# Performance work log

Hardware: AMD Instinct MI355X
Metric: run time of the kernel (lower is better)

The kernel has to match this reference:

```python
import jax, jax.numpy as jnp
import numpy as np
import math

N, LQ, D, H, L, P, DFF, NL = 16, 300, 256, 8, 3, 4, 1024, 6
TLENS = (4096, 2048, 1024)
T = sum(TLENS)
TEMP = 10000.0

def _ln(x, g, b, eps=1e-5):
    m = x.mean(-1, keepdims=True)
    v = ((x - m) ** 2).mean(-1, keepdims=True)
    return (x - m) * jax.lax.rsqrt(v + eps) * g + b

def _mlp2(x, w0, b0, w1, b1):
    return jax.nn.relu(x @ w0.T + b0) @ w1.T + b1

def _sine_embed(ref):
    # ref: (N, LQ, 2) (center, width) -> (N, LQ, 2*D)
    dim_t = TEMP ** (2.0 * (jnp.arange(D) // 2) / D)
    p = ref * (2.0 * math.pi)
    def inter(v):
        return jnp.stack([jnp.sin(v[..., 0::2]), jnp.cos(v[..., 1::2])], -1).reshape(v.shape[:-1] + (-1,))
    pc = p[..., 0:1] / dim_t
    pw = p[..., 1:2] / dim_t
    return jnp.concatenate([inter(pc), inter(pw)], -1)

def _mha(q, k, v, in_w, in_b, out_w, out_b):
    Nb, Lq, Dm = q.shape
    Dh = Dm // H
    wq, wk, wv = jnp.split(in_w, 3, 0)
    bq, bk, bv = jnp.split(in_b, 3, 0)
    qh = (q @ wq.T + bq).reshape(Nb, Lq, H, Dh)
    kh = (k @ wk.T + bk).reshape(Nb, Lq, H, Dh)
    vh = (v @ wv.T + bv).reshape(Nb, Lq, H, Dh)
    att = jax.nn.softmax(jnp.einsum('nqhd,nkhd->nhqk', qh, kh) / math.sqrt(Dh), -1)
    o = jnp.einsum('nhqk,nkhd->nqhd', att, vh).reshape(Nb, Lq, Dm)
    return o @ out_w.T + out_b

def _deform_attn(q, ref, src, pad_mask, t_lens, start, ow, ob, aww, awb, vw, vb, pw, pb):
    # q: (N,LQ,D); ref: (N,LQ,L,2) normalized (center,width); src: (N,T,D)
    Nb, Lq, Dm = q.shape
    Dh = Dm // H
    val = (src @ vw.T + vb) * (~pad_mask)[..., None]
    val = val.reshape(Nb, -1, H, Dh).transpose(0, 2, 1, 3)  # (N,H,T,Dh)
    off = (q @ ow.T + ob).reshape(Nb, Lq, H, L, P)
    aw = jax.nn.softmax((q @ aww.T + awb).reshape(Nb, Lq, H, L * P), -1).reshape(Nb, Lq, H, L, P)
    # 1-D deformable sampling locations: center + offset/P * width * 0.5
    loc = ref[:, :, None, :, 0, None] + off / P * ref[:, :, None, :, 1, None] * 0.5  # (N,LQ,H,L,P)
    tl = t_lens[None, None, None, :, None]
    x = loc * tl.astype(loc.dtype) - 0.5  # align_corners=False linear sampling
    x0f = jnp.floor(x)
    f = x - x0f
    x0 = x0f.astype(jnp.int32)
    m0 = (x0 >= 0) & (x0 < tl)
    m1 = (x0 + 1 >= 0) & (x0 + 1 < tl)
    st = start[None, None, None, :, None]
    i0 = st + jnp.clip(x0, 0, tl - 1)
    i1 = st + jnp.clip(x0 + 1, 0, tl - 1)
    def tr(a):
        return a.transpose(0, 2, 1, 3, 4).reshape(Nb, H, Lq * L * P)
    g0 = jnp.take_along_axis(val, tr(i0)[..., None], axis=2)  # (N,H,M,Dh)
    g1 = jnp.take_along_axis(val, tr(i1)[..., None], axis=2)
    samp = g0 * ((1.0 - tr(f)) * tr(m0))[..., None] + g1 * (tr(f) * tr(m1))[..., None]
    samp = samp.reshape(Nb, H, Lq, L * P, Dh)
    w = tr(aw).reshape(Nb, H, Lq, L * P)
    o = jnp.einsum('nhqk,nhqkd->nqhd', w, samp).reshape(Nb, Lq, Dm)
    return o @ pw.T + pb

def _forward(tgt, enc_output_segments, feature_durations, src, src_valid_ratios,
             grid_w0, grid_b0, grid_w1, grid_b1, qs_w0, qs_b0, qs_w1, qs_b1,
             sa_in_w, sa_in_b, sa_out_w, sa_out_b,
             n1_g, n1_b, n2_g, n2_b, n3_g, n3_b,
             off_w, off_b, aw_w, aw_b, val_w, val_b, outp_w, outp_b,
             ffn_w1, ffn_b1, ffn_w2, ffn_b2,
             temporal_lens, level_start_index, src_padding_mask):
    seg = jax.lax.stop_gradient(enc_output_segments)  # original detaches proposals
    ref = jnp.stack([seg[..., 0], jnp.exp(seg[..., 1])], -1)  # (N,LQ,2) center,width
    out = tgt
    for l in range(NL):
        ref_in = (ref / feature_durations[:, None, None])[:, :, None, :] * src_valid_ratios[:, None, :, None]
        sine = _sine_embed(ref)
        raw_qpos = _mlp2(sine, grid_w0, grid_b0, grid_w1, grid_b1)
        qpos = _mlp2(out, qs_w0, qs_b0, qs_w1, qs_b1) * raw_qpos
        q = out + qpos
        out = _ln(out + _mha(q, q, out, sa_in_w[l], sa_in_b[l], sa_out_w[l], sa_out_b[l]), n1_g[l], n1_b[l])
        ca = _deform_attn(out + qpos, ref_in, src, src_padding_mask, temporal_lens, level_start_index,
                          off_w[l], off_b[l], aw_w[l], aw_b[l], val_w[l], val_b[l], outp_w[l], outp_b[l])
        out = _ln(out + ca, n2_g[l], n2_b[l])
        ff = jax.nn.relu(out @ ffn_w1[l].T + ffn_b1[l]) @ ffn_w2[l].T + ffn_b2[l]
        out = _ln(out + ff, n3_g[l], n3_b[l])
    return out

def setup_inputs():
    key = jax.random.key(0)
    ks = iter(jax.random.split(key, 64))
    def nrm(shape, s=0.02):
        return (s * jax.random.normal(next(ks), shape)).astype(jnp.float32)
    dur = 64.0
    inp = {}
    inp['tgt'] = nrm((N, LQ, D), 1.0)
    c = jax.random.uniform(next(ks), (N, LQ)) * dur
    w = jnp.log(jax.random.uniform(next(ks), (N, LQ)) * 4.0 + 0.5)
    inp['enc_output_segments'] = jnp.stack([c, w], -1)
    inp['feature_durations'] = jnp.full((N,), dur, jnp.float32)
    inp['src'] = nrm((N, T, D), 1.0)
    inp['temporal_lens'] = jnp.array(TLENS, jnp.int32)
    inp['level_start_index'] = jnp.array(np.cumsum((0,) + TLENS[:-1]), jnp.int32)
    inp['src_valid_ratios'] = jnp.ones((N, L), jnp.float32)
    inp['src_padding_mask'] = jnp.zeros((N, T), bool)
    inp['grid_w0'] = nrm((D, 2 * D)); inp['grid_b0'] = jnp.zeros((D,))
    inp['grid_w1'] = nrm((D, D)); inp['grid_b1'] = jnp.zeros((D,))
    inp['qs_w0'] = nrm((D, D)); inp['qs_b0'] = jnp.zeros((D,))
    inp['qs_w1'] = nrm((D, D)); inp['qs_b1'] = jnp.zeros((D,))
    inp['sa_in_w'] = nrm((NL, 3 * D, D)); inp['sa_in_b'] = jnp.zeros((NL, 3 * D))
    inp['sa_out_w'] = nrm((NL, D, D)); inp['sa_out_b'] = jnp.zeros((NL, D))
    for nm in ('n1', 'n2', 'n3'):
        inp[nm + '_g'] = jnp.ones((NL, D)); inp[nm + '_b'] = jnp.zeros((NL, D))
    inp['off_w'] = nrm((NL, H * L * P, D))
    inp['off_b'] = (jax.random.uniform(next(ks), (NL, H * L * P)) * 2.0 - 1.0) * P
    inp['aw_w'] = nrm((NL, H * L * P, D)); inp['aw_b'] = jnp.zeros((NL, H * L * P))
    inp['val_w'] = nrm((NL, D, D)); inp['val_b'] = jnp.zeros((NL, D))
    inp['outp_w'] = nrm((NL, D, D)); inp['outp_b'] = jnp.zeros((NL, D))
    inp['ffn_w1'] = nrm((NL, DFF, D)); inp['ffn_b1'] = jnp.zeros((NL, DFF))
    inp['ffn_w2'] = nrm((NL, D, DFF)); inp['ffn_b2'] = jnp.zeros((NL, D))
    return inp

def reference(tgt, enc_output_segments, feature_durations, src, temporal_lens, level_start_index,
              src_valid_ratios, src_padding_mask,
              grid_w0, grid_b0, grid_w1, grid_b1, qs_w0, qs_b0, qs_w1, qs_b1,
              sa_in_w, sa_in_b, sa_out_w, sa_out_b,
              n1_g, n1_b, n2_g, n2_b, n3_g, n3_b,
              off_w, off_b, aw_w, aw_b, val_w, val_b, outp_w, outp_b,
              ffn_w1, ffn_b1, ffn_w2, ffn_b2):
    return _forward(tgt, enc_output_segments, feature_durations, src, src_valid_ratios,
                    grid_w0, grid_b0, grid_w1, grid_b1, qs_w0, qs_b0, qs_w1, qs_b1,
                    sa_in_w, sa_in_b, sa_out_w, sa_out_b,
                    n1_g, n1_b, n2_g, n2_b, n3_g, n3_b,
                    off_w, off_b, aw_w, aw_b, val_w, val_b, outp_w, outp_b,
                    ffn_w1, ffn_b1, ffn_w2, ffn_b2,
                    temporal_lens, level_start_index, src_padding_mask)
```

## Files before the change

kernel.cpp:

```cpp
#include <hip/hip_runtime.h>
#include <cstdint>

#define NB   16
#define LQN  300
#define DM   256
#define NH   8
#define DH   32
#define NLV  3
#define DFFN 1024
#define NLAY 6
#define TT   7168
#define MROW (NB*LQN)
#define SROW (NB*TT)

typedef __attribute__((ext_vector_type(8))) short bf16x8;
typedef __attribute__((ext_vector_type(4))) float f32x4;

__device__ __forceinline__ float bf2f(short u) {
  unsigned x = ((unsigned)(unsigned short)u) << 16;
  return __builtin_bit_cast(float, x);
}
__device__ __forceinline__ short f2bf(float f) {
  unsigned u = __builtin_bit_cast(unsigned, f);
  u += 0x7fffu + ((u >> 16) & 1u);
  return (short)(u >> 16);
}
__device__ __forceinline__ void load_lds16(const void* g, void* l) {
  __builtin_amdgcn_global_load_lds(
      (const __attribute__((address_space(1))) unsigned int*)g,
      (__attribute__((address_space(3))) unsigned int*)l, 16, 0, 0);
}
#define MFMA(a,b,c) __builtin_amdgcn_mfma_f32_16x16x32_bf16((a),(b),(c),0,0,0)

struct CvtPtrs { const float* p[13]; };

__global__ __launch_bounds__(256)
void cvt_all_kernel(CvtPtrs ptrs, short* __restrict__ dst)
{
  const long gid = (long)blockIdx.x*256 + threadIdx.x;
  const long cums[14] = {0,32768,49152,65536,81920,376832,475136,512000,
                         548864,647168,745472,1138688,1531904,8871936};
  int s = 0;
  #pragma unroll
  for (int i = 1; i < 13; ++i) s += (gid >= cums[i]) ? 1 : 0;
  const long rel = gid - cums[s];
  const float4 v = ((const float4*)ptrs.p[s])[rel];
  long dstIdx = gid;
  if (s == 6) { const long l = rel/6144, w = rel%6144; dstIdx = 475136 + l*12288 + w; }
  else if (s == 7) { const long l = rel/6144, w = rel%6144; dstIdx = 475136 + l*12288 + 6144 + w; }
  ((short4*)dst)[dstIdx] = make_short4(f2bf(v.x), f2bf(v.y), f2bf(v.z), f2bf(v.w));
}

#define VLS 264

__global__ __launch_bounds__(512, 1)
void val_gemm(const short* __restrict__ srcbf, const short* __restrict__ Bw,
              const float* __restrict__ bias, short* __restrict__ Cb,
              const unsigned char* __restrict__ rowmask)
{
  __shared__ short Bs[256*VLS];
  const int tid = threadIdx.x, wid = tid >> 6, lane = tid & 63;
  const int fr = lane & 15, fq = lane >> 4;

  for (int t = tid; t < 8192; t += 512) {
    const int row = t >> 5, ch = t & 31;
    const int chs = ch ^ ((row >> 4) & 7);
    *(bf16x8*)&Bs[row*VLS + chs*8] = *(const bf16x8*)(Bw + row*256 + ch*8);
  }
  __syncthreads();

  float bv[16];
  #pragma unroll
  for (int j = 0; j < 4; ++j)
    *(float4*)&bv[j*4] = *(const float4*)(bias + fr*16 + j*4);

  const int rbase = (blockIdx.x*8 + wid) * 32;

  bf16x8 a[2][8];
  #pragma unroll
  for (int h = 0; h < 2; ++h)
    #pragma unroll
    for (int ks = 0; ks < 8; ++ks)
      a[h][ks] = *(const bf16x8*)(srcbf + (long)(rbase + h*16 + fr)*256 + ks*32 + fq*8);

  f32x4 acc[2][16] = {};
  #pragma unroll
  for (int ks = 0; ks < 8; ++ks) {
    #pragma unroll
    for (int nt = 0; nt < 16; ++nt) {
      const bf16x8 b = *(const bf16x8*)&Bs[(fr*16 + nt)*VLS + (((ks*4 + fq) ^ (fr & 7)))*8];
      acc[0][nt] = MFMA(a[0][ks], b, acc[0][nt]);
      acc[1][nt] = MFMA(a[1][ks], b, acc[1][nt]);
    }
  }

  #pragma unroll
  for (int h = 0; h < 2; ++h) {
    #pragma unroll
    for (int r = 0; r < 4; ++r) {
      const int grow = rbase + h*16 + fq*4 + r;
      const float msc = rowmask[grow] ? 0.0f : 1.0f;
      bf16x8 o0, o1;
      #pragma unroll
      for (int j = 0; j < 8; ++j) {
        o0[j] = f2bf((acc[h][j][r]   + bv[j])   * msc);
        o1[j] = f2bf((acc[h][8+j][r] + bv[8+j]) * msc);
      }
      short* cp = Cb + (long)grow*256 + fr*16;
      *(bf16x8*)cp       = o0;
      *(bf16x8*)(cp + 8) = o1;
    }
  }
}

template<int EPI>
__global__ __launch_bounds__(256)
void gemm64(const short* __restrict__ A, const short* __restrict__ B,
            const float* __restrict__ bias, const float* __restrict__ bias2,
            float* __restrict__ Cf, short* __restrict__ Cb, short* __restrict__ Cb2,
            int M, int N, int K, int ldc,
            const float* __restrict__ rawq, const float* __restrict__ resid)
{
  __shared__ short As[2][64*64];
  __shared__ short Bs[2][64*64];
  const int tid = threadIdx.x, wid = tid >> 6, lane = tid & 63;
  const int wr = wid >> 1, wc = wid & 1;
  const int fr = lane & 15, fq = lane >> 4;
  const int bm = blockIdx.x, bn = blockIdx.y;
  const int lrow = lane >> 3;
  const int schk = ((lane & 7) ^ lrow) * 8;
  const int nk = K >> 6;

  f32x4 acc[2][2] = {};

  auto stg = [&](int kt, int bsel) {
    const int k0 = kt << 6;
    #pragma unroll
    for (int i = 0; i < 2; ++i) {
      const int rr = wid*16 + i*8 + lrow;
      load_lds16(A + (long)(bm*64 + rr)*K + k0 + schk, &As[bsel][(wid*16 + i*8)*64]);
      load_lds16(B + (long)(bn*64 + rr)*K + k0 + schk, &Bs[bsel][(wid*16 + i*8)*64]);
    }
  };

  stg(0, 0);
  for (int t = 0; t < nk; ++t) {
    const int cur = t & 1;
    if (t + 1 < nk) {
      stg(t + 1, cur ^ 1);
      asm volatile("s_waitcnt vmcnt(4)" ::: "memory");
    } else {
      asm volatile("s_waitcnt vmcnt(0)" ::: "memory");
    }
    __builtin_amdgcn_s_barrier();
    __builtin_amdgcn_sched_barrier(0);
    #pragma unroll
    for (int kk = 0; kk < 64; kk += 32) {
      bf16x8 af[2], bv[2];
      #pragma unroll
      for (int mi = 0; mi < 2; ++mi)
        af[mi] = *(const bf16x8*)&As[cur][(wr*32 + mi*16 + fr)*64 + (((kk>>3)+fq) ^ (fr&7))*8];
      #pragma unroll
      for (int ni = 0; ni < 2; ++ni)
        bv[ni] = *(const bf16x8*)&Bs[cur][(wc*32 + ni*16 + fr)*64 + (((kk>>3)+fq) ^ (fr&7))*8];
      #pragma unroll
      for (int mi = 0; mi < 2; ++mi)
        #pragma unroll
        for (int ni = 0; ni < 2; ++ni)
          acc[mi][ni] = MFMA(af[mi], bv[ni], acc[mi][ni]);
    }
    __builtin_amdgcn_s_barrier();
  }

  #pragma unroll
  for (int mi = 0; mi < 2; ++mi) {
    #pragma unroll
    for (int r = 0; r < 4; ++r) {
      const int grow = bm*64 + wr*32 + mi*16 + fq*4 + r;
      #pragma unroll
      for (int ni = 0; ni < 2; ++ni) {
        const int gcol = bn*64 + wc*32 + ni*16 + fr;
        float v = acc[mi][ni][r];
        if (EPI == 4) v += (gcol < 96) ? bias[gcol] : bias2[gcol-96];
        else v += bias[gcol];
        const long off = (long)grow*ldc + gcol;
        if (EPI == 0) {
          if (Cf) Cf[off] = v;
          if (Cb) Cb[off] = f2bf(v);
        } else if (EPI == 1) {
          Cb[off] = f2bf(fmaxf(v, 0.0f));
        } else if (EPI == 2) {
          const float qp = v * rawq[off];
          Cf[off] = qp;
          Cb[off] = f2bf(resid[off] + qp);
        } else if (EPI == 4) {
          Cf[off] = v;
        }
      }
    }
  }
}

__global__ __launch_bounds__(256)
void ew0_kernel(const float* __restrict__ tgt, float* __restrict__ out, short* __restrict__ outbf)
{
  const long i = (long)blockIdx.x*256 + threadIdx.x;
  const float4 v = ((const float4*)tgt)[i];
  ((float4*)out)[i] = v;
  ((short4*)outbf)[i] = make_short4(f2bf(v.x), f2bf(v.y), f2bf(v.z), f2bf(v.w));
}

__global__ __launch_bounds__(256)
void init_ref_kernel(const float* __restrict__ seg, const float* __restrict__ dur,
                     const float* __restrict__ valid,
                     short* __restrict__ sinebf, float* __restrict__ refin)
{
  const int m = blockIdx.x;
  const int n = m / LQN;
  const int t = threadIdx.x;
  const float c = seg[(long)m*2 + 0];
  const float w = __expf(seg[(long)m*2 + 1]);
  const float e = (float)(t & ~1) * (1.0f/256.0f);
  const float invdim = __expf(-e * 9.2103403719761836f);
  const float twopi = 6.2831853071795864f;
  const float a0 = c * twopi * invdim;
  const float a1 = w * twopi * invdim;
  const float v0 = (t & 1) ? cosf(a0) : sinf(a0);
  const float v1 = (t & 1) ? cosf(a1) : sinf(a1);
  sinebf[(long)m*512 + t]       = f2bf(v0);
  sinebf[(long)m*512 + 256 + t] = f2bf(v1);
  if (t < 6) {
    const int l = t >> 1, cc = t & 1;
    const float rv = cc ? w : c;
    refin[(long)m*6 + l*2 + cc] = rv / dur[n] * valid[n*NLV + l];
  }
}

#define KPAD 320
#define KSTR 40
#define VSTR 328
#define PSTR 328

__global__ __launch_bounds__(256)
void attn_mfma(const short* __restrict__ qk, const short* __restrict__ vv,
               short* __restrict__ outb)
{
  __shared__ short Kl[KPAD*KSTR];
  __shared__ short Vt[DH*VSTR];
  __shared__ short Pl[4][16*PSTR];
  const int b = blockIdx.x;
  const int half = b & 1, h = (b >> 1) & 7, n = b >> 4;
  const int tid = threadIdx.x, wid = tid >> 6, lane = tid & 63;
  const int fr = lane & 15, fq = lane >> 4;

  const short* qkn = qk + (long)n*LQN*512;
  const short* vn  = vv + (long)n*LQN*256;

  for (int t = tid; t < KPAD*4; t += 256) {
    const int r = t >> 2, c = t & 3;
    bf16x8 kv = {}, vw = {};
    if (r < LQN) {
      kv = *(const bf16x8*)(qkn + (long)r*512 + 256 + h*32 + c*8);
      vw = *(const bf16x8*)(vn  + (long)r*256 + h*32 + c*8);
    }
    *(bf16x8*)&Kl[r*KSTR + c*8] = kv;
    #pragma unroll
    for (int j = 0; j < 8; ++j) Vt[(c*8+j)*VSTR + r] = vw[j];
  }
  for (int t = tid; t < 4*16*24; t += 256) {
    const int w = t / (16*24), rr = (t / 24) & 15, cc = t % 24;
    Pl[w][rr*PSTR + 304 + cc] = 0;
  }
  __syncthreads();

  const int tlo = half ? 10 : 0, thi = half ? 19 : 10;
  const float scl2 = 0.17677669529663687f * 1.4426950408889634f;

  for (int qt = tlo + wid; qt < thi; qt += 4) {
    const int q0 = qt * 16;
    const int qrow = min(q0 + fr, LQN-1);
    const bf16x8 qf = *(const bf16x8*)(qkn + (long)qrow*512 + h*32 + fq*8);
    f32x4 s[19];
    #pragma unroll
    for (int t = 0; t < 19; ++t) {
      const bf16x8 kf = *(const bf16x8*)&Kl[(t*16+fr)*KSTR + fq*8];
      s[t] = MFMA(qf, kf, ((f32x4){0.f,0.f,0.f,0.f}));
    }
    float mx[4] = {-3e38f,-3e38f,-3e38f,-3e38f};
    #pragma unroll
    for (int t = 0; t < 19; ++t) {
      const bool valid = (t < 18) || (fr < 12);
      #pragma unroll
      for (int r = 0; r < 4; ++r) if (valid) mx[r] = fmaxf(mx[r], s[t][r]);
    }
    #pragma unroll
    for (int r = 0; r < 4; ++r) {
      #pragma unroll
      for (int o = 1; o < 16; o <<= 1) mx[r] = fmaxf(mx[r], __shfl_xor(mx[r], o));
      mx[r] *= scl2;
    }
    float l[4] = {0.f,0.f,0.f,0.f};
    #pragma unroll
    for (int t = 0; t < 19; ++t) {
      const bool valid = (t < 18) || (fr < 12);
      #pragma unroll
      for (int r = 0; r < 4; ++r) {
        const float p = valid ? exp2f(s[t][r]*scl2 - mx[r]) : 0.0f;
        l[r] += p;
        Pl[wid][(fq*4+r)*PSTR + t*16 + fr] = f2bf(p);
      }
    }
    #pragma unroll
    for (int r = 0; r < 4; ++r) {
      #pragma unroll
      for (int o = 1; o < 16; o <<= 1) l[r] += __shfl_xor(l[r], o);
    }
    f32x4 o0 = {}, o1 = {};
    #pragma unroll
    for (int ck = 0; ck < 10; ++ck) {
      const bf16x8 pf = *(const bf16x8*)&Pl[wid][fr*PSTR + ck*32 + fq*8];
      const bf16x8 v0 = *(const bf16x8*)&Vt[fr*VSTR + ck*32 + fq*8];
      const bf16x8 v1 = *(const bf16x8*)&Vt[(16+fr)*VSTR + ck*32 + fq*8];
      o0 = MFMA(pf, v0, o0);
      o1 = MFMA(pf, v1, o1);
    }
    #pragma unroll
    for (int r = 0; r < 4; ++r) {
      const int qq = q0 + fq*4 + r;
      if (qq < LQN) {
        const float inv = 1.0f / l[r];
        outb[((long)(n*LQN+qq))*256 + h*32 + fr]      = f2bf(o0[r]*inv);
        outb[((long)(n*LQN+qq))*256 + h*32 + 16 + fr] = f2bf(o1[r]*inv);
      }
    }
  }
}

__global__ __launch_bounds__(256)
void ln_kernel(const float* __restrict__ resid, const float* __restrict__ delta,
               const float* __restrict__ g, const float* __restrict__ b,
               float* __restrict__ of, short* __restrict__ ob,
               const float* __restrict__ qpos, short* __restrict__ caqb)
{
  const int m = blockIdx.x, c = threadIdx.x;
  const long idx = (long)m*DM + c;
  const float x = resid[idx] + delta[idx];
  float s = x, s2 = x*x;
  #pragma unroll
  for (int o = 1; o < 64; o <<= 1) { s += __shfl_xor(s, o); s2 += __shfl_xor(s2, o); }
  __shared__ float rs[4], rs2[4];
  const int w = c >> 6;
  if ((c & 63) == 0) { rs[w] = s; rs2[w] = s2; }
  __syncthreads();
  s  = rs[0]+rs[1]+rs[2]+rs[3];
  s2 = rs2[0]+rs2[1]+rs2[2]+rs2[3];
  const float mean = s * (1.0f/DM);
  const float var  = s2 * (1.0f/DM) - mean*mean;
  const float y = (x - mean) * rsqrtf(var + 1e-5f) * g[c] + b[c];
  of[idx] = y;
  if (ob) ob[idx] = f2bf(y);
  if (qpos) caqb[idx] = f2bf(y + qpos[idx]);
}

__global__ __launch_bounds__(256)
void sample_kernel(const short* __restrict__ val, int ldv,
                   const float* __restrict__ offaw, const float* __restrict__ refin,
                   const int* __restrict__ tlens, const int* __restrict__ lstart,
                   short* __restrict__ cab)
{
  const int m = blockIdx.x;
  const int n = m / LQN;
  const int tid = threadIdx.x;
  __shared__ int2  lI[96];
  __shared__ float2 lW[96];
  if ((tid & 31) == 0) {
    const int h = tid >> 5;
    const float* row = offaw + (long)m*192;
    float aw[12];
    float mx = -1e30f;
    #pragma unroll
    for (int lp = 0; lp < 12; ++lp) { aw[lp] = row[96 + h*12 + lp]; mx = fmaxf(mx, aw[lp]); }
    float sum = 0.0f;
    #pragma unroll
    for (int lp = 0; lp < 12; ++lp) { aw[lp] = __expf(aw[lp]-mx); sum += aw[lp]; }
    const float invs = 1.0f / sum;
    #pragma unroll
    for (int lp = 0; lp < 12; ++lp) {
      const int l = lp >> 2;
      const int tli = tlens[l];
      const float off = row[h*12 + lp];
      const float loc = refin[(long)m*6 + l*2] + off * 0.25f * refin[(long)m*6 + l*2 + 1] * 0.5f;
      const float x = loc * (float)tli - 0.5f;
      const float x0f = floorf(x);
      const float f = x - x0f;
      const int x0 = (int)x0f;
      const int i0 = lstart[l] + min(max(x0,   0), tli-1);
      const int i1 = lstart[l] + min(max(x0+1, 0), tli-1);
      const float wgt = aw[lp]*invs;
      const float w0 = (x0   >= 0 && x0   < tli) ? wgt*(1.0f-f) : 0.0f;
      const float w1 = (x0+1 >= 0 && x0+1 < tli) ? wgt*f        : 0.0f;
      lI[h*12 + lp] = make_int2(i0, i1);
      lW[h*12 + lp] = make_float2(w0, w1);
    }
  }
  __syncthreads();
  const int h = tid >> 5;
  const short* vb = val + (long)n*TT*ldv;
  float acc = 0.0f;
  #pragma unroll
  for (int lp = 0; lp < 12; ++lp) {
    const int e = h*12 + lp;
    const int2 ii = lI[e];
    const float2 ww = lW[e];
    acc += ww.x * bf2f(vb[(long)ii.x*ldv + tid]) + ww.y * bf2f(vb[(long)ii.y*ldv + tid]);
  }
  cab[(long)m*DM + tid] = f2bf(acc);
}

static inline void g64(hipStream_t st, int epi, const short* A, const short* B,
                       const float* bias, const float* bias2,
                       float* Cf, short* Cb, short* Cb2,
                       int M, int N, int K, int ldc,
                       const float* rawq = nullptr, const float* resid = nullptr)
{
  dim3 g(M/64, N/64), blk(256);
  switch (epi) {
    case 0: gemm64<0><<<g,blk,0,st>>>(A,B,bias,bias2,Cf,Cb,Cb2,M,N,K,ldc,rawq,resid); break;
    case 1: gemm64<1><<<g,blk,0,st>>>(A,B,bias,bias2,Cf,Cb,Cb2,M,N,K,ldc,rawq,resid); break;
    case 2: gemm64<2><<<g,blk,0,st>>>(A,B,bias,bias2,Cf,Cb,Cb2,M,N,K,ldc,rawq,resid); break;
    default:gemm64<4><<<g,blk,0,st>>>(A,B,bias,bias2,Cf,Cb,Cb2,M,N,K,ldc,rawq,resid); break;
  }
}

extern "C" void kernel_launch(void* const* d_in, const int* in_sizes, int n_in,
                              void* d_out, int out_size, void* d_ws, size_t ws_size,
                              hipStream_t stream)
{
  const float* tgt    = (const float*)d_in[0];
  const float* seg    = (const float*)d_in[1];
  const float* dur    = (const float*)d_in[2];
  const float* src    = (const float*)d_in[3];
  const int*   tlens  = (const int*)d_in[4];
  const int*   lstart = (const int*)d_in[5];
  const float* valid  = (const float*)d_in[6];
  const unsigned char* pmask = (const unsigned char*)d_in[7];
  const float* grid_w0 = (const float*)d_in[8];
  const float* grid_b0 = (const float*)d_in[9];
  const float* grid_w1 = (const float*)d_in[10];
  const float* grid_b1 = (const float*)d_in[11];
  const float* qs_w0 = (const float*)d_in[12];
  const float* qs_b0 = (const float*)d_in[13];
  const float* qs_w1 = (const float*)d_in[14];
  const float* qs_b1 = (const float*)d_in[15];
  const float* sa_in_w  = (const float*)d_in[16];
  const float* sa_in_b  = (const float*)d_in[17];
  const float* sa_out_w = (const float*)d_in[18];
  const float* sa_out_b = (const float*)d_in[19];
  const float* n1_g = (const float*)d_in[20];
  const float* n1_b = (const float*)d_in[21];
  const float* n2_g = (const float*)d_in[22];
  const float* n2_b = (const float*)d_in[23];
  const float* n3_g = (const float*)d_in[24];
  const float* n3_b = (const float*)d_in[25];
  const float* off_w = (const float*)d_in[26];
  const float* off_b = (const float*)d_in[27];
  const float* aw_w  = (const float*)d_in[28];
  const float* aw_b  = (const float*)d_in[29];
  const float* val_w = (const float*)d_in[30];
  const float* val_b = (const float*)d_in[31];
  const float* outp_w = (const float*)d_in[32];
  const float* outp_b = (const float*)d_in[33];
  const float* ffn_w1 = (const float*)d_in[34];
  const float* ffn_b1 = (const float*)d_in[35];
  const float* ffn_w2 = (const float*)d_in[36];
  const float* ffn_b2 = (const float*)d_in[37];

  const long W_G0=0, W_G1=131072, W_QS0=196608, W_QS1=262144, W_SAIN=327680,
             W_SAOUT=1507328, W_OFFAW=1900544, W_VAL=2195456,
             W_OUTP=2588672, W_FFN1=2981888, W_FFN2=4554752, W_SRC=6127616;

  char* ws = (char*)d_ws;
  short* wbf    = (short*)(ws + 0);
  short* srcbf  = wbf + W_SRC;
  short* sinebf = (short*)(ws + 70975488);
  short* ghbf   = (short*)(ws + 75890688);
  float* rawq   = (float*)(ws + 78348288);
  float* out    = (float*)(ws + 83263488);
  short* qbf    = (short*)(ws + 88178688);
  short* outbf  = qbf + (long)MROW*DM;
  short* t1bf   = (short*)(ws + 93093888);
  float* qpos   = (float*)(ws + 95551488);
  short* qkbf   = (short*)(ws + 100466688);
  short* vbf    = (short*)(ws + 105381888);
  short* attnbf = (short*)(ws + 107839488);
  float* tmpf   = (float*)(ws + 110297088);
  short* caqb   = (short*)(ws + 115212288);
  float* offaw  = (float*)(ws + 117669888);
  short* cabf   = (short*)(ws + 128729088);
  short* ffnhbf = (short*)(ws + 131186688);
  float* refin  = (float*)(ws + 141017088);
  short* valbf  = (short*)(ws + 141132288);

  CvtPtrs cp;
  cp.p[0]=grid_w0; cp.p[1]=grid_w1; cp.p[2]=qs_w0; cp.p[3]=qs_w1; cp.p[4]=sa_in_w;
  cp.p[5]=sa_out_w; cp.p[6]=off_w; cp.p[7]=aw_w; cp.p[8]=val_w; cp.p[9]=outp_w;
  cp.p[10]=ffn_w1; cp.p[11]=ffn_w2; cp.p[12]=src;
  cvt_all_kernel<<<dim3(34656), dim3(256), 0, stream>>>(cp, wbf);

  ew0_kernel<<<dim3(1200), dim3(256), 0, stream>>>(tgt, out, outbf);
  init_ref_kernel<<<dim3(MROW), dim3(256), 0, stream>>>(seg, dur, valid, sinebf, refin);

  g64(stream, 1, sinebf, wbf + W_G0, grid_b0, nullptr, nullptr, ghbf, nullptr, MROW, 256, 512, 256);
  g64(stream, 0, ghbf,   wbf + W_G1, grid_b1, nullptr, rawq, nullptr, nullptr, MROW, 256, 256, 256);

  for (int l = 0; l < NLAY; ++l) {
    g64(stream, 1, outbf, wbf + W_QS0, qs_b0, nullptr, nullptr, t1bf, nullptr, MROW, 256, 256, 256);
    g64(stream, 2, t1bf,  wbf + W_QS1, qs_b1, nullptr, qpos, qbf, nullptr, MROW, 256, 256, 256,
        rawq, out);
    g64(stream, 0, qbf, wbf + W_SAIN + (long)l*196608, sa_in_b + l*768, nullptr,
        nullptr, qkbf, nullptr, MROW, 512, 256, 512);
    g64(stream, 0, outbf, wbf + W_SAIN + (long)l*196608 + 131072, sa_in_b + l*768 + 512, nullptr,
        nullptr, vbf, nullptr, MROW, 256, 256, 256);
    attn_mfma<<<dim3(256), dim3(256), 0, stream>>>(qkbf, vbf, attnbf);
    g64(stream, 0, attnbf, wbf + W_SAOUT + (long)l*65536, sa_out_b + l*256, nullptr,
        tmpf, nullptr, nullptr, MROW, 256, 256, 256);
    ln_kernel<<<dim3(MROW), dim3(256), 0, stream>>>(out, tmpf, n1_g + l*256, n1_b + l*256,
                                                    out, outbf, qpos, caqb);
    g64(stream, 4, caqb, wbf + W_OFFAW + (long)l*49152, off_b + l*96, aw_b + l*96,
        offaw, nullptr, nullptr, MROW, 192, 256, 192);
    val_gemm<<<dim3(448), dim3(512), 0, stream>>>(
        srcbf, wbf + W_VAL + (long)l*65536, val_b + l*256, valbf, pmask);
    sample_kernel<<<dim3(MROW), dim3(256), 0, stream>>>(
        valbf, 256, offaw, refin, tlens, lstart, cabf);
    g64(stream, 0, cabf, wbf + W_OUTP + (long)l*65536, outp_b + l*256, nullptr,
        tmpf, nullptr, nullptr, MROW, 256, 256, 256);
    ln_kernel<<<dim3(MROW), dim3(256), 0, stream>>>(out, tmpf, n2_g + l*256, n2_b + l*256,
                                                    out, outbf, nullptr, nullptr);
    g64(stream, 1, outbf, wbf + W_FFN1 + (long)l*262144, ffn_b1 + l*1024, nullptr,
        nullptr, ffnhbf, nullptr, MROW, 1024, 256, 1024);
    g64(stream, 0, ffnhbf, wbf + W_FFN2 + (long)l*262144, ffn_b2 + l*256, nullptr,
        tmpf, nullptr, nullptr, MROW, 256, 1024, 256);
    float* of = (l == NLAY-1) ? (float*)d_out : out;
    ln_kernel<<<dim3(MROW), dim3(256), 0, stream>>>(out, tmpf, n3_g + l*256, n3_b + l*256,
                                                    of, outbf, nullptr, nullptr);
  }
}
```

Baseline: 996.3 us.

## Replace K=256 GEMMs with weight-stationary LDS kernel holding full B slice

Adds an sgemm kernel that loads a whole 256-column by 256-K weight slice into shared memory once per block. Each wave then computes a 16-row strip with A held in registers and writes vectorized epilogues. All K=256 projections move to this kernel, while the K=512/1024 GEMMs stay on a simplified gemm64. The aim is to cut the repeated K-loop staging and barriers and to widen stores. In exchange it uses large LDS (about 128KB+ per block), gives one block per CU, and needs many accumulator registers.

```diff
diff --git a/kernel.cpp b/kernel.cpp
--- a/kernel.cpp
+++ b/kernel.cpp
@@ -114,12 +114,120 @@
 }
 
 template<int EPI>
+__global__ __launch_bounds__(512, 1)
+void sgemm(const short* __restrict__ A, const short* __restrict__ Bw,
+           const float* __restrict__ bias, const float* __restrict__ bias2,
+           float* __restrict__ Cf, short* __restrict__ Cb,
+           int M, int NR, int ldc,
+           const float* __restrict__ rawq, const float* __restrict__ resid)
+{
+  __shared__ short Bs[256*VLS];
+  const int tid = threadIdx.x, wid = tid >> 6, lane = tid & 63;
+  const int fr = lane & 15, fq = lane >> 4;
+  const int coff = blockIdx.y * 256;
+
+  for (int t = tid; t < NR*32; t += 512) {
+    const int row = t >> 5, ch = t & 31;
+    const int chs = ch ^ ((row >> 4) & 7);
+    *(bf16x8*)&Bs[row*VLS + chs*8] = *(const bf16x8*)(Bw + (long)(coff + row)*256 + ch*8);
+  }
+  __syncthreads();
+
+  const int s = blockIdx.x*8 + wid;
+  if (s*16 >= M) return;
+  const int rbase = s*16;
+  const bool colok = (fr*16 < NR);
+
+  float bv[16];
+  if (colok) {
+    #pragma unroll
+    for (int j = 0; j < 16; ++j) {
+      const int gc = coff + fr*16 + j;
+      if (EPI == 4) bv[j] = (gc < 96) ? bias[gc] : bias2[gc - 96];
+      else          bv[j] = bias[gc];
+    }
+  } else {
+    #pragma unroll
+    for (int j = 0; j < 16; ++j) bv[j] = 0.0f;
+  }
+
+  bf16x8 a[8];
+  #pragma unroll
+  for (int ks = 0; ks < 8; ++ks)
+    a[ks] = *(const bf16x8*)(A + (long)(rbase + fr)*256 + ks*32 + fq*8);
+
+  f32x4 acc[16] = {};
+  #pragma unroll
+  for (int ks = 0; ks < 8; ++ks)
+    #pragma unroll
+    for (int nt = 0; nt < 16; ++nt) {
+      const bf16x8 b = *(const bf16x8*)&Bs[(fr*16 + nt)*VLS + (((ks*4 + fq) ^ (fr & 7)))*8];
+      acc[nt] = MFMA(a[ks], b, acc[nt]);
+    }
+
+  if (!colok) return;
+
+  #pragma unroll
+  for (int r = 0; r < 4; ++r) {
+    const int grow = rbase + fq*4 + r;
+    const long off = (long)grow*ldc + coff + fr*16;
+    float y[16];
+    #pragma unroll
+    for (int nt = 0; nt < 16; ++nt) y[nt] = acc[nt][r] + bv[nt];
+
+    if (EPI == 0) {
+      if (Cf) {
+        #pragma unroll
+        for (int j = 0; j < 4; ++j) *(float4*)(Cf + off + j*4) = *(const float4*)&y[j*4];
+      }
+      if (Cb) {
+        bf16x8 o0, o1;
+        #pragma unroll
+        for (int j = 0; j < 8; ++j) { o0[j] = f2bf(y[j]); o1[j] = f2bf(y[8+j]); }
+        *(bf16x8*)(Cb + off) = o0;
+        *(bf16x8*)(Cb + off + 8) = o1;
+      }
+    } else if (EPI == 1) {
+      bf16x8 o0, o1;
+      #pragma unroll
+      for (int j = 0; j < 8; ++j) {
+        o0[j] = f2bf(fmaxf(y[j],   0.0f));
+        o1[j] = f2bf(fmaxf(y[8+j], 0.0f));
+      }
+      *(bf16x8*)(Cb + off) = o0;
+      *(bf16x8*)(Cb + off + 8) = o1;
+    } else if (EPI == 2) {
+      float rq[16], rs[16];
+      #pragma unroll
+      for (int j = 0; j < 4; ++j) {
+        *(float4*)&rq[j*4] = *(const float4*)(rawq  + off + j*4);
+        *(float4*)&rs[j*4] = *(const float4*)(resid + off + j*4);
+      }
+      bf16x8 o0, o1;
+      #pragma unroll
+      for (int j = 0; j < 16; ++j) {
+        const float qp = y[j] * rq[j];
+        y[j] = qp;
+        const short b = f2bf(rs[j] + qp);
+        if (j < 8) o0[j] = b; else o1[j-8] = b;
+      }
+      #pragma unroll
+      for (int j = 0; j < 4; ++j) *(float4*)(Cf + off + j*4) = *(const float4*)&y[j*4];
+      *(bf16x8*)(Cb + off) = o0;
+      *(bf16x8*)(Cb + off + 8) = o1;
+    } else {
+      #pragma unroll
+      for (int j = 0; j < 4; ++j) *(float4*)(Cf + off + j*4) = *(const float4*)&y[j*4];
+    }
+  }
+}
+
+template<int EPI>
 __global__ __launch_bounds__(256)
 void gemm64(const short* __restrict__ A, const short* __restrict__ B,
-            const float* __restrict__ bias, const float* __restrict__ bias2,
-            float* __restrict__ Cf, short* __restrict__ Cb, short* __restrict__ Cb2,
-            int M, int N, int K, int ldc,
-            const float* __restrict__ rawq, const float* __restrict__ resid)
+            const float* __restrict__ bias,
+            float* __restrict__ Cf, short* __restrict__ Cb,
+            int M, int N, int K, int ldc)
 {
   __shared__ short As[2][64*64];
   __shared__ short Bs[2][64*64];
@@ -180,22 +288,10 @@
       #pragma unroll
       for (int ni = 0; ni < 2; ++ni) {
         const int gcol = bn*64 + wc*32 + ni*16 + fr;
-        float v = acc[mi][ni][r];
-        if (EPI == 4) v += (gcol < 96) ? bias[gcol] : bias2[gcol-96];
-        else v += bias[gcol];
+        const float v = acc[mi][ni][r] + bias[gcol];
         const long off = (long)grow*ldc + gcol;
-        if (EPI == 0) {
-          if (Cf) Cf[off] = v;
-          if (Cb) Cb[off] = f2bf(v);
-        } else if (EPI == 1) {
-          Cb[off] = f2bf(fmaxf(v, 0.0f));
-        } else if (EPI == 2) {
-          const float qp = v * rawq[off];
-          Cf[off] = qp;
-          Cb[off] = f2bf(resid[off] + qp);
-        } else if (EPI == 4) {
-          Cf[off] = v;
-        }
+        if (EPI == 0) Cf[off] = v;
+        else Cb[off] = f2bf(fmaxf(v, 0.0f));
       }
     }
   }
@@ -417,18 +513,17 @@
   cab[(long)m*DM + tid] = f2bf(acc);
 }
 
-static inline void g64(hipStream_t st, int epi, const short* A, const short* B,
-                       const float* bias, const float* bias2,
-                       float* Cf, short* Cb, short* Cb2,
-                       int M, int N, int K, int ldc,
-                       const float* rawq = nullptr, const float* resid = nullptr)
-{
-  dim3 g(M/64, N/64), blk(256);
+static inline void sg(hipStream_t st, int epi, const short* A, const short* B,
+                      const float* bias, const float* bias2,
+                      float* Cf, short* Cb, int M, int NR, int nbn, int ldc,
+                      const float* rawq = nullptr, const float* resid = nullptr)
+{
+  dim3 g((M/16 + 7)/8, nbn), blk(512);
   switch (epi) {
-    case 0: gemm64<0><<<g,blk,0,st>>>(A,B,bias,bias2,Cf,Cb,Cb2,M,N,K,ldc,rawq,resid); break;
-    case 1: gemm64<1><<<g,blk,0,st>>>(A,B,bias,bias2,Cf,Cb,Cb2,M,N,K,ldc,rawq,resid); break;
-    case 2: gemm64<2><<<g,blk,0,st>>>(A,B,bias,bias2,Cf,Cb,Cb2,M,N,K,ldc,rawq,resid); break;
-    default:gemm64<4><<<g,blk,0,st>>>(A,B,bias,bias2,Cf,Cb,Cb2,M,N,K,ldc,rawq,resid); break;
+    case 0: sgemm<0><<<g,blk,0,st>>>(A,B,bias,bias2,Cf,Cb,M,NR,ldc,rawq,resid); break;
+    case 1: sgemm<1><<<g,blk,0,st>>>(A,B,bias,bias2,Cf,Cb,M,NR,ldc,rawq,resid); break;
+    case 2: sgemm<2><<<g,blk,0,st>>>(A,B,bias,bias2,Cf,Cb,M,NR,ldc,rawq,resid); break;
+    default:sgemm<4><<<g,blk,0,st>>>(A,B,bias,bias2,Cf,Cb,M,NR,ldc,rawq,resid); break;
   }
 }
 
@@ -510,36 +605,38 @@
   ew0_kernel<<<dim3(1200), dim3(256), 0, stream>>>(tgt, out, outbf);
   init_ref_kernel<<<dim3(MROW), dim3(256), 0, stream>>>(seg, dur, valid, sinebf, refin);
 
-  g64(stream, 1, sinebf, wbf + W_G0, grid_b0, nullptr, nullptr, ghbf, nullptr, MROW, 256, 512, 256);
-  g64(stream, 0, ghbf,   wbf + W_G1, grid_b1, nullptr, rawq, nullptr, nullptr, MROW, 256, 256, 256);
+  gemm64<1><<<dim3(75,4), dim3(256), 0, stream>>>(sinebf, wbf + W_G0, grid_b0,
+                                                  nullptr, ghbf, MROW, 256, 512, 256);
+  sg(stream, 0, ghbf, wbf + W_G1, grid_b1, nullptr, rawq, nullptr, MROW, 256, 1, 256);
 
   for (int l = 0; l < NLAY; ++l) {
-    g64(stream, 1, outbf, wbf + W_QS0, qs_b0, nullptr, nullptr, t1bf, nullptr, MROW, 256, 256, 256);
-    g64(stream, 2, t1bf,  wbf + W_QS1, qs_b1, nullptr, qpos, qbf, nullptr, MROW, 256, 256, 256,
-        rawq, out);
-    g64(stream, 0, qbf, wbf + W_SAIN + (long)l*196608, sa_in_b + l*768, nullptr,
-        nullptr, qkbf, nullptr, MROW, 512, 256, 512);
-    g64(stream, 0, outbf, wbf + W_SAIN + (long)l*196608 + 131072, sa_in_b + l*768 + 512, nullptr,
-        nullptr, vbf, nullptr, MROW, 256, 256, 256);
+    sg(stream, 1, outbf, wbf + W_QS0, qs_b0, nullptr, nullptr, t1bf, MROW, 256, 1, 256);
+    sg(stream, 2, t1bf,  wbf + W_QS1, qs_b1, nullptr, qpos, qbf, MROW, 256, 1, 256,
+       rawq, out);
+    sg(stream, 0, qbf, wbf + W_SAIN + (long)l*196608, sa_in_b + l*768, nullptr,
+       nullptr, qkbf, MROW, 256, 2, 512);
+    sg(stream, 0, outbf, wbf + W_SAIN + (long)l*196608 + 131072, sa_in_b + l*768 + 512, nullptr,
+       nullptr, vbf, MROW, 256, 1, 256);
     attn_mfma<<<dim3(256), dim3(256), 0, stream>>>(qkbf, vbf, attnbf);
-    g64(stream, 0, attnbf, wbf + W_SAOUT + (long)l*65536, sa_out_b + l*256, nullptr,
-        tmpf, nullptr, nullptr, MROW, 256, 256, 256);
+    sg(stream, 0, attnbf, wbf + W_SAOUT + (long)l*65536, sa_out_b + l*256, nullptr,
+       tmpf, nullptr, MROW, 256, 1, 256);
     ln_kernel<<<dim3(MROW), dim3(256), 0, stream>>>(out, tmpf, n1_g + l*256, n1_b + l*256,
                                                     out, outbf, qpos, caqb);
-    g64(stream, 4, caqb, wbf + W_OFFAW + (long)l*49152, off_b + l*96, aw_b + l*96,
-        offaw, nullptr, nullptr, MROW, 192, 256, 192);
+    sg(stream, 4, caqb, wbf + W_OFFAW + (long)l*49152, off_b + l*96, aw_b + l*96,
+       offaw, nullptr, MROW, 192, 1, 192);
     val_gemm<<<dim3(448), dim3(512), 0, stream>>>(
         srcbf, wbf + W_VAL + (long)l*65536, val_b + l*256, valbf, pmask);
     sample_kernel<<<dim3(MROW), dim3(256), 0, stream>>>(
         valbf, 256, offaw, refin, tlens, lstart, cabf);
-    g64(stream, 0, cabf, wbf + W_OUTP + (long)l*65536, outp_b + l*256, nullptr,
-        tmpf, nullptr, nullptr, MROW, 256, 256, 256);
+    sg(stream, 0, cabf, wbf + W_OUTP + (long)l*65536, outp_b + l*256, nullptr,
+       tmpf, nullptr, MROW, 256, 1, 256);
     ln_kernel<<<dim3(MROW), dim3(256), 0, stream>>>(out, tmpf, n2_g + l*256, n2_b + l*256,
                                                     out, outbf, nullptr, nullptr);
-    g64(stream, 1, outbf, wbf + W_FFN1 + (long)l*262144, ffn_b1 + l*1024, nullptr,
-        nullptr, ffnhbf, nullptr, MROW, 1024, 256, 1024);
-    g64(stream, 0, ffnhbf, wbf + W_FFN2 + (long)l*262144, ffn_b2 + l*256, nullptr,
-        tmpf, nullptr, nullptr, MROW, 256, 1024, 256);
+    sg(stream, 1, outbf, wbf + W_FFN1 + (long)l*262144, ffn_b1 + l*1024, nullptr,
+       nullptr, ffnhbf, MROW, 256, 4, 1024);
+    gemm64<0><<<dim3(75,4), dim3(256), 0, stream>>>(ffnhbf, wbf + W_FFN2 + (long)l*262144,
+                                                    ffn_b2 + l*256, tmpf, nullptr,
+                                                    MROW, 256, 1024, 256);
     float* of = (l == NLAY-1) ? (float*)d_out : out;
     ln_kernel<<<dim3(MROW), dim3(256), 0, stream>>>(out, tmpf, n3_g + l*256, n3_b + l*256,
                                                     of, outbf, nullptr, nullptr);
```

Result: slower. 1.415 ms (+42.1%).

## Split value GEMM over two column halves and stream A fragments per k-step

Applied to the files above, without the earlier changes.

The value-projection GEMM now gives each block 128 of the 256 output columns, with a second grid dimension. This halves the shared-memory weight tile and the accumulator registers, which lets two blocks share a CU. The A operand is no longer preloaded in full; it is double-buffered one k-step ahead to cut register pressure. The cost is that every A row is now read from global memory twice, once per column half, and the weight tile is loaded twice as many times.

```diff
diff --git a/kernel.cpp b/kernel.cpp
--- a/kernel.cpp
+++ b/kernel.cpp
@@ -53,45 +53,49 @@
 
 #define VLS 264
 
-__global__ __launch_bounds__(512, 1)
+__global__ __launch_bounds__(512, 2)
 void val_gemm(const short* __restrict__ srcbf, const short* __restrict__ Bw,
               const float* __restrict__ bias, short* __restrict__ Cb,
               const unsigned char* __restrict__ rowmask)
 {
-  __shared__ short Bs[256*VLS];
+  __shared__ short Bs[128*VLS];
   const int tid = threadIdx.x, wid = tid >> 6, lane = tid & 63;
   const int fr = lane & 15, fq = lane >> 4;
-
-  for (int t = tid; t < 8192; t += 512) {
+  const int coff = blockIdx.y * 128;
+
+  for (int t = tid; t < 4096; t += 512) {
     const int row = t >> 5, ch = t & 31;
     const int chs = ch ^ ((row >> 4) & 7);
-    *(bf16x8*)&Bs[row*VLS + chs*8] = *(const bf16x8*)(Bw + row*256 + ch*8);
+    *(bf16x8*)&Bs[row*VLS + chs*8] = *(const bf16x8*)(Bw + (long)(coff + row)*256 + ch*8);
   }
   __syncthreads();
 
-  float bv[16];
-  #pragma unroll
-  for (int j = 0; j < 4; ++j)
-    *(float4*)&bv[j*4] = *(const float4*)(bias + fr*16 + j*4);
+  float bv[8];
+  #pragma unroll
+  for (int j = 0; j < 2; ++j)
+    *(float4*)&bv[j*4] = *(const float4*)(bias + coff + fr*8 + j*4);
 
   const int rbase = (blockIdx.x*8 + wid) * 32;
 
-  bf16x8 a[2][8];
-  #pragma unroll
-  for (int h = 0; h < 2; ++h)
-    #pragma unroll
-    for (int ks = 0; ks < 8; ++ks)
-      a[h][ks] = *(const bf16x8*)(srcbf + (long)(rbase + h*16 + fr)*256 + ks*32 + fq*8);
-
-  f32x4 acc[2][16] = {};
+  bf16x8 ac0, ac1, an0, an1;
+  ac0 = *(const bf16x8*)(srcbf + (long)(rbase + fr)*256 + fq*8);
+  ac1 = *(const bf16x8*)(srcbf + (long)(rbase + 16 + fr)*256 + fq*8);
+
+  f32x4 acc[2][8] = {};
   #pragma unroll
   for (int ks = 0; ks < 8; ++ks) {
-    #pragma unroll
-    for (int nt = 0; nt < 16; ++nt) {
-      const bf16x8 b = *(const bf16x8*)&Bs[(fr*16 + nt)*VLS + (((ks*4 + fq) ^ (fr & 7)))*8];
-      acc[0][nt] = MFMA(a[0][ks], b, acc[0][nt]);
-      acc[1][nt] = MFMA(a[1][ks], b, acc[1][nt]);
-    }
+    if (ks < 7) {
+      an0 = *(const bf16x8*)(srcbf + (long)(rbase + fr)*256 + (ks+1)*32 + fq*8);
+      an1 = *(const bf16x8*)(srcbf + (long)(rbase + 16 + fr)*256 + (ks+1)*32 + fq*8);
+    }
+    #pragma unroll
+    for (int nt = 0; nt < 8; ++nt) {
+      const int row = fr*8 + nt;
+      const bf16x8 b = *(const bf16x8*)&Bs[row*VLS + (((ks*4 + fq) ^ ((row >> 4) & 7)))*8];
+      acc[0][nt] = MFMA(ac0, b, acc[0][nt]);
+      acc[1][nt] = MFMA(ac1, b, acc[1][nt]);
+    }
+    if (ks < 7) { ac0 = an0; ac1 = an1; }
   }
 
   #pragma unroll
@@ -100,15 +104,10 @@
     for (int r = 0; r < 4; ++r) {
       const int grow = rbase + h*16 + fq*4 + r;
       const float msc = rowmask[grow] ? 0.0f : 1.0f;
-      bf16x8 o0, o1;
-      #pragma unroll
-      for (int j = 0; j < 8; ++j) {
-        o0[j] = f2bf((acc[h][j][r]   + bv[j])   * msc);
-        o1[j] = f2bf((acc[h][8+j][r] + bv[8+j]) * msc);
-      }
-      short* cp = Cb + (long)grow*256 + fr*16;
-      *(bf16x8*)cp       = o0;
-      *(bf16x8*)(cp + 8) = o1;
+      bf16x8 o;
+      #pragma unroll
+      for (int j = 0; j < 8; ++j) o[j] = f2bf((acc[h][j][r] + bv[j]) * msc);
+      *(bf16x8*)(Cb + (long)grow*256 + coff + fr*8) = o;
     }
   }
 }
@@ -528,7 +527,7 @@
                                                     out, outbf, qpos, caqb);
     g64(stream, 4, caqb, wbf + W_OFFAW + (long)l*49152, off_b + l*96, aw_b + l*96,
         offaw, nullptr, nullptr, MROW, 192, 256, 192);
-    val_gemm<<<dim3(448), dim3(512), 0, stream>>>(
+    val_gemm<<<dim3(448, 2), dim3(512), 0, stream>>>(
         srcbf, wbf + W_VAL + (long)l*65536, val_b + l*256, valbf, pmask);
     sample_kernel<<<dim3(MROW), dim3(256), 0, stream>>>(
         valbf, 256, offaw, refin, tlens, lstart, cabf);
```

Measured after the change: 973.0 us (median of 2 runs). 1.02x faster.
